# Kernel optimization log

Measured on AMD Instinct MI355X. Metric: run time of the kernel, lower is better.

The kernel has to match this reference:

```python
import jax, jax.numpy as jnp
import numpy as np
import math

HEAD_DIM = 128
DEPTH = 12
LAMBDA_INIT = 0.8 - 0.6 * math.exp(-0.3 * DEPTH)
EPS = 1e-5
SCALE = 1.0 / math.sqrt(HEAD_DIM / 2)


def setup_inputs() -> dict:
    key = jax.random.key(0)
    ks = jax.random.split(key, 8)
    b, t, d = 2, 4096, 2048
    return {
        "x": jax.random.normal(ks[0], (b, t, d), dtype=jnp.float32),
        "wq": jax.random.normal(ks[1], (d, HEAD_DIM), dtype=jnp.float32) * 0.02,
        "wk": jax.random.normal(ks[2], (d, HEAD_DIM), dtype=jnp.float32) * 0.02,
        "wv": jax.random.normal(ks[3], (d, HEAD_DIM), dtype=jnp.float32) * 0.02,
        "lambda_q1": jax.random.normal(ks[4], (HEAD_DIM // 2,), dtype=jnp.float32) * 0.1,
        "lambda_q2": jax.random.normal(ks[5], (HEAD_DIM // 2,), dtype=jnp.float32) * 0.1,
        "lambda_k1": jax.random.normal(ks[6], (HEAD_DIM // 2,), dtype=jnp.float32) * 0.1,
        "lambda_k2": jax.random.normal(ks[7], (HEAD_DIM // 2,), dtype=jnp.float32) * 0.1,
        "ln_weight": jnp.ones((HEAD_DIM,), dtype=jnp.float32),
    }


def reference(x, wq, wk, wv, lambda_q1, lambda_q2, lambda_k1, lambda_k2, ln_weight):
    b, t, d = x.shape
    q = x @ wq  # [b,t,hd]
    k = x @ wk
    v = x @ wv
    h = HEAD_DIM // 2
    q1, q2 = q[..., :h], q[..., h:]
    k1, k2 = k[..., :h], k[..., h:]
    # causal mask: True where attention is disallowed (strictly upper triangle)
    causal = jnp.triu(jnp.ones((t, t), dtype=bool), k=1)
    neg_inf = jnp.float32(-jnp.inf)

    def masked_softmax(qh, kh):
        scores = jnp.einsum('btd,bsd->bts', qh, kh) * SCALE
        scores = jnp.where(causal, neg_inf, scores)
        return jax.nn.softmax(scores, axis=-1)

    a1 = masked_softmax(q1, k1)
    a2 = masked_softmax(q2, k2)
    lmbda = (jnp.exp(jnp.sum(lambda_q1 * lambda_k1))
             - jnp.exp(jnp.sum(lambda_q2 * lambda_k2))
             + LAMBDA_INIT)
    diffattn = jnp.einsum('bts,bsd->btd', a1 - lmbda * a2, v)
    rms = jnp.sqrt(jnp.mean(diffattn * diffattn, axis=-1, keepdims=True) + EPS)
    out = (1.0 - LAMBDA_INIT) * (diffattn / rms * ln_weight)
    return out
```

## Files before the change

### kernel.cpp

```cpp
#include <hip/hip_runtime.h>
#include <stdint.h>

#define T_SEQ 4096
#define NB 2
#define D_MODEL 2048
#define HD 128

typedef __attribute__((ext_vector_type(4)))  float f32x4;
typedef __attribute__((ext_vector_type(16))) float f32x16;
typedef __attribute__((ext_vector_type(8)))  short bf16x8;
typedef __attribute__((ext_vector_type(4)))  unsigned u32x4;

#define LAMBDA_INIT 0.7836057665316244f
#define OUT_SCALE   0.21639423346837556f

__device__ __forceinline__ unsigned short f2bf(float f) {
  unsigned int u = __float_as_uint(f);
  u += 0x7FFFu + ((u >> 16) & 1u);
  return (unsigned short)(u >> 16);
}
__device__ __forceinline__ float bf2f(unsigned short h) {
  return __uint_as_float(((unsigned int)h) << 16);
}
__device__ __forceinline__ unsigned cvt_pk_bf16(float a, float b) {
  unsigned r;
  asm("v_cvt_pk_bf16_f32 %0, %1, %2" : "=v"(r) : "v"(a), "v"(b));
  return r;
}
__device__ __forceinline__ void gload16(const void* g, void* l) {
  __builtin_amdgcn_global_load_lds(
      (const __attribute__((address_space(1))) unsigned int*)g,
      (__attribute__((address_space(3))) unsigned int*)l, 16, 0, 0);
}

__global__ __launch_bounds__(256) void wtrans(
    const float* __restrict__ wq, const float* __restrict__ wk,
    const float* __restrict__ wv, unsigned short* __restrict__ wT)
{
  const int which = blockIdx.y;
  const int s = blockIdx.x;
  const float* w = (which == 0) ? wq : ((which == 1) ? wk : wv);
  const float scale = (which == 0) ? 0.125f : 1.0f;
  const int tid = threadIdx.x;
  #pragma unroll
  for (int j = 0; j < 4; ++j) {
    int cell = j * 256 + tid;
    int q = cell >> 7, n = cell & 127;
    int kb = s * 64 + q * 8;
    float v[8];
    #pragma unroll
    for (int e = 0; e < 8; ++e) v[e] = w[(size_t)(kb + e) * HD + n] * scale;
    u32x4 pk = { cvt_pk_bf16(v[0], v[1]), cvt_pk_bf16(v[2], v[3]),
                 cvt_pk_bf16(v[4], v[5]), cvt_pk_bf16(v[6], v[7]) };
    *reinterpret_cast<u32x4*>(&wT[(size_t)(which * 32 + s) * 8192 + (size_t)cell * 8]) = pk;
  }
}

__global__ __launch_bounds__(512, 1) void qkv_part(
    const float* __restrict__ x, const unsigned short* __restrict__ wT,
    float* __restrict__ P)
{
  __shared__ __align__(16) char lds[4][32768];
  const int tid = threadIdx.x, lane = tid & 63, wid = tid >> 6;
  const int bid = blockIdx.x;
  const int ks = bid & 1;
  const int mt = bid >> 1;
  const int wm = wid >> 1, wn = wid & 1;
  const int fr = lane & 15, fq = lane >> 4;
  const int m0 = mt * 64;

  const float* xbase = x + (size_t)m0 * D_MODEL + ks * 1024;
  const unsigned short* wbase = wT + (size_t)(ks * 16) * 8192;

  f32x4 acc[3][4];
  #pragma unroll
  for (int ty = 0; ty < 3; ++ty)
    #pragma unroll
    for (int j = 0; j < 4; ++j) acc[ty][j] = (f32x4){0.f, 0.f, 0.f, 0.f};

#define DMA(t) do {                                                        \
    char* As_ = &lds[(t) & 3][0];                                          \
    char* Bs_ = &lds[(t) & 3][8192];                                       \
    const int k0_ = (t) * 32;                                              \
    {                                                                      \
      int c = wid * 64 + lane;                                             \
      int row = c >> 3, kcp = c & 7;                                       \
      gload16(xbase + (size_t)row * D_MODEL + k0_ + ((kcp ^ (row & 7)) << 2), \
              As_ + wid * 1024);                                           \
    }                                                                      \
    _Pragma("unroll")                                                      \
    for (int ty = 0; ty < 3; ++ty) {                                       \
      const unsigned short* bs_ = wbase + (size_t)ty * 262144              \
                                + (size_t)((t) >> 1) * 8192                \
                                + (size_t)((t) & 1) * 4096;                \
      gload16(bs_ + (size_t)wid * 512 + (size_t)lane * 8,                  \
              Bs_ + (size_t)ty * 8192 + wid * 1024);                       \
    }                                                                      \
  } while (0)

#define STEP(t, VMIMM) do {                                                \
    asm volatile("s_waitcnt vmcnt(" VMIMM ")" ::: "memory");               \
    __builtin_amdgcn_s_barrier();                                          \
    __builtin_amdgcn_sched_barrier(0);                                     \
    if ((t) + 3 < 32) DMA((t) + 3);                                        \
    __builtin_amdgcn_sched_barrier(0);                                     \
    const char* Ac_ = &lds[(t) & 3][0];                                    \
    const char* Bc_ = &lds[(t) & 3][8192];                                 \
    bf16x8 af_;                                                            \
    {                                                                      \
      int row = wm * 16 + fr;                                              \
      int p1 = (2 * fq) ^ (row & 7), p2 = (2 * fq + 1) ^ (row & 7);        \
      f32x4 lo = *reinterpret_cast<const f32x4*>(Ac_ + (row * 8 + p1) * 16); \
      f32x4 hi = *reinterpret_cast<const f32x4*>(Ac_ + (row * 8 + p2) * 16); \
      u32x4 pk = { cvt_pk_bf16(lo[0], lo[1]), cvt_pk_bf16(lo[2], lo[3]),   \
                   cvt_pk_bf16(hi[0], hi[1]), cvt_pk_bf16(hi[2], hi[3]) }; \
      af_ = *reinterpret_cast<bf16x8*>(&pk);                               \
    }                                                                      \
    _Pragma("unroll")                                                      \
    for (int ty = 0; ty < 3; ++ty)                                         \
      _Pragma("unroll")                                                    \
      for (int ni = 0; ni < 4; ++ni) {                                     \
        int n = wn * 64 + ni * 16 + fr;                                    \
        bf16x8 bf_ = *reinterpret_cast<const bf16x8*>(                     \
            Bc_ + (size_t)ty * 8192 + (fq * 128 + n) * 16);                \
        acc[ty][ni] = __builtin_amdgcn_mfma_f32_16x16x32_bf16(af_, bf_, acc[ty][ni], 0, 0, 0); \
      }                                                                    \
  } while (0)

  DMA(0); DMA(1); DMA(2);
  #pragma unroll 1
  for (int t = 0; t < 30; ++t) STEP(t, "8");
  STEP(30, "4");
  STEP(31, "0");
#undef STEP
#undef DMA

  #pragma unroll
  for (int ty = 0; ty < 3; ++ty) {
    float* pp = P + ((size_t)(ks * 3 + ty) * 8192 + m0) * 128;
    #pragma unroll
    for (int ni = 0; ni < 4; ++ni)
      #pragma unroll
      for (int r = 0; r < 4; ++r)
        pp[(size_t)(wm * 16 + fq * 4 + r) * 128 + wn * 64 + ni * 16 + fr]
            = acc[ty][ni][r];
  }
}

__global__ __launch_bounds__(256) void qkv_merge(
    const float* __restrict__ P,
    unsigned short* __restrict__ qb, unsigned short* __restrict__ kS,
    unsigned short* __restrict__ vS)
{
  const int gid = blockIdx.x * 256 + threadIdx.x;
  const size_t e8 = (size_t)gid * 8;
  const int type = (int)(e8 >> 20);
  const int rem  = (int)(e8 & 1048575);
  const int m = rem >> 7, n0 = rem & 127;
  const float* p0 = P + (size_t)type * 1048576 + rem;
  const float* p1 = p0 + (size_t)3 * 1048576;
  f32x4 a0 = *reinterpret_cast<const f32x4*>(p0);
  f32x4 a1 = *reinterpret_cast<const f32x4*>(p0 + 4);
  f32x4 b0 = *reinterpret_cast<const f32x4*>(p1);
  f32x4 b1 = *reinterpret_cast<const f32x4*>(p1 + 4);
  float s[8];
  #pragma unroll
  for (int j = 0; j < 4; ++j) { s[j] = a0[j] + b0[j]; s[4 + j] = a1[j] + b1[j]; }
  u32x4 pk = { cvt_pk_bf16(s[0], s[1]), cvt_pk_bf16(s[2], s[3]),
               cvt_pk_bf16(s[4], s[5]), cvt_pk_bf16(s[6], s[7]) };

  const int bb = m >> 12, tt = m & 4095;
  const int kt = tt >> 5, kvl = tt & 31;
  if (type == 0) {
    *reinterpret_cast<u32x4*>(&qb[(size_t)m * HD + n0]) = pk;
  } else if (type == 1) {
    int g = n0 >> 6, hl = n0 & 63;
    int ksf = hl >> 4, r8 = (hl >> 3) & 1;
    size_t idx = ((((((size_t)bb * 128 + kt) * 2 + g) * 4) + ksf) << 9)
               + (size_t)(kvl + 32 * r8) * 8;
    *reinterpret_cast<u32x4*>(&kS[idx]) = pk;
  } else {
    int f = kvl >> 4, r8v = (kvl >> 3) & 1, e = kvl & 7;
    #pragma unroll
    for (int j = 0; j < 8; ++j) {
      int n = n0 + j;
      int vcb = n >> 5;
      size_t idx = (((((size_t)bb * 128 + kt) * 8) + vcb * 2 + f) << 9)
                 + (size_t)((n & 31) + 32 * r8v) * 8 + e;
      vS[idx] = f2bf(s[j]);
    }
  }
}

template<int LOG2S>
__global__ __launch_bounds__(256, 2) void diff_attn_part(
    const unsigned short* __restrict__ qb, const unsigned short* __restrict__ kS,
    const unsigned short* __restrict__ vS,
    unsigned short* __restrict__ po, float* __restrict__ pm, float* __restrict__ pl)
{
  constexpr int S = 1 << LOG2S;
  const int tid = threadIdx.x, lane = tid & 63, wid = tid >> 6;
  const int wave_id = blockIdx.x * 4 + wid;
  const int sp = wave_id & (S - 1);
  const int g  = (wave_id >> LOG2S) & 1;
  const int qt_raw = (wave_id >> (LOG2S + 1)) & 127;
  const int b  = wave_id >> (LOG2S + 8);
  const int qt = 127 - qt_raw;
  const int slot = (((b * 128 + qt) * 2 + g) << LOG2S) + sp;
  const int lq = lane & 31, lh = lane >> 5;
  const int q0 = qt * 32;
  const int n  = qt + 1;
  const int kt0 = (n * sp) >> LOG2S;
  const int kt1 = (n * (sp + 1)) >> LOG2S;

  bf16x8 qf[4];
  const unsigned short* qp = qb + ((size_t)b * T_SEQ + q0 + lq) * HD + g * 64 + lh * 8;
  #pragma unroll
  for (int ks = 0; ks < 4; ++ks) qf[ks] = *reinterpret_cast<const bf16x8*>(qp + ks * 16);

  f32x16 acc[4];
  #pragma unroll
  for (int v = 0; v < 4; ++v)
    #pragma unroll
    for (int r = 0; r < 16; ++r) acc[v][r] = 0.f;
  float mrun = -1e30f, lrun = 0.f;

  const unsigned short* kbase = kS + ((size_t)(b * 128) * 2 + g) * 4 * 512 + lane * 8;
  const unsigned short* vbase = vS + (size_t)(b * 128) * 8 * 512 + lane * 8;
  #define KFRAG(kt, ks) (kbase + ((size_t)(kt) * 8 + (ks)) * 512)
  #define VFRAG(kt, f)  (vbase + ((size_t)(kt) * 8 + (f)) * 512)

  bf16x8 kf[4];
  if (kt0 < kt1) {
    #pragma unroll
    for (int ks = 0; ks < 4; ++ks)
      kf[ks] = *reinterpret_cast<const bf16x8*>(KFRAG(kt0, ks));
  }

  for (int kt = kt0; kt < kt1; ++kt) {
    bf16x8 vfa[4], vfb[4];
    #pragma unroll
    for (int vcb = 0; vcb < 4; ++vcb) {
      vfa[vcb] = *reinterpret_cast<const bf16x8*>(VFRAG(kt, vcb * 2));
      vfb[vcb] = *reinterpret_cast<const bf16x8*>(VFRAG(kt, vcb * 2 + 1));
    }
    bf16x8 kfn[4];
    const bool more = (kt + 1 < kt1);
    if (more) {
      #pragma unroll
      for (int ks = 0; ks < 4; ++ks)
        kfn[ks] = *reinterpret_cast<const bf16x8*>(KFRAG(kt + 1, ks));
    }
    f32x16 sc;
    #pragma unroll
    for (int r = 0; r < 16; ++r) sc[r] = 0.f;
    #pragma unroll
    for (int ks = 0; ks < 4; ++ks)
      sc = __builtin_amdgcn_mfma_f32_32x32x16_bf16(kf[ks], qf[ks], sc, 0, 0, 0);

    float p[16];
    if (kt == n - 1) {
      #pragma unroll
      for (int r = 0; r < 16; ++r) {
        int rloc = (r & 3) + 8 * (r >> 2) + 4 * lh;
        p[r] = (rloc > lq) ? -1e30f : sc[r];
      }
    } else {
      #pragma unroll
      for (int r = 0; r < 16; ++r) p[r] = sc[r];
    }
    float t16[16];
    #pragma unroll
    for (int r = 0; r < 16; ++r) t16[r] = p[r];
    #pragma unroll
    for (int st = 8; st >= 1; st >>= 1)
      #pragma unroll
      for (int r = 0; r < 8; ++r)
        if (r < st) t16[r] = fmaxf(t16[r], t16[r + st]);
    float pmax = fmaxf(t16[0], __shfl_xor(t16[0], 32));
    if (__any(pmax > mrun + 8.f)) {
      float mn = fmaxf(mrun, pmax);
      float al = __expf(mrun - mn);
      lrun *= al;
      #pragma unroll
      for (int v = 0; v < 4; ++v)
        #pragma unroll
        for (int r = 0; r < 16; ++r) acc[v][r] *= al;
      mrun = mn;
    }
    float psum;
    {
      float s16[16];
      #pragma unroll
      for (int r = 0; r < 16; ++r) { p[r] = __expf(p[r] - mrun); s16[r] = p[r]; }
      #pragma unroll
      for (int st = 8; st >= 1; st >>= 1)
        #pragma unroll
        for (int r = 0; r < 8; ++r)
          if (r < st) s16[r] += s16[r + st];
      psum = s16[0];
    }
    lrun += psum + __shfl_xor(psum, 32);

    unsigned A0 = cvt_pk_bf16(p[0],  p[1]),  A1 = cvt_pk_bf16(p[2],  p[3]);
    unsigned A2 = cvt_pk_bf16(p[4],  p[5]),  A3 = cvt_pk_bf16(p[6],  p[7]);
    unsigned A4 = cvt_pk_bf16(p[8],  p[9]),  A5 = cvt_pk_bf16(p[10], p[11]);
    unsigned A6 = cvt_pk_bf16(p[12], p[13]), A7 = cvt_pk_bf16(p[14], p[15]);
    unsigned pA0 = (unsigned)__shfl_xor((int)A0, 32);
    unsigned pA1 = (unsigned)__shfl_xor((int)A1, 32);
    unsigned pA2 = (unsigned)__shfl_xor((int)A2, 32);
    unsigned pA3 = (unsigned)__shfl_xor((int)A3, 32);
    unsigned pA4 = (unsigned)__shfl_xor((int)A4, 32);
    unsigned pA5 = (unsigned)__shfl_xor((int)A5, 32);
    unsigned pA6 = (unsigned)__shfl_xor((int)A6, 32);
    unsigned pA7 = (unsigned)__shfl_xor((int)A7, 32);
    u32x4 w0, w1;
    w0[0] = lh ? pA2 : A0;  w0[1] = lh ? pA3 : A1;
    w0[2] = lh ? A2  : pA0; w0[3] = lh ? A3  : pA1;
    w1[0] = lh ? pA6 : A4;  w1[1] = lh ? pA7 : A5;
    w1[2] = lh ? A6  : pA4; w1[3] = lh ? A7  : pA5;
    bf16x8 pb0 = *reinterpret_cast<bf16x8*>(&w0);
    bf16x8 pb1 = *reinterpret_cast<bf16x8*>(&w1);
    #pragma unroll
    for (int vcb = 0; vcb < 4; ++vcb) {
      acc[vcb] = __builtin_amdgcn_mfma_f32_32x32x16_bf16(vfa[vcb], pb0, acc[vcb], 0, 0, 0);
      acc[vcb] = __builtin_amdgcn_mfma_f32_32x32x16_bf16(vfb[vcb], pb1, acc[vcb], 0, 0, 0);
    }
    if (more) {
      #pragma unroll
      for (int ks = 0; ks < 4; ++ks) kf[ks] = kfn[ks];
    }
  }
  #undef KFRAG
  #undef VFRAG
  const size_t pbase = (size_t)slot * (HD * 32);
  #pragma unroll
  for (int vcb = 0; vcb < 4; ++vcb)
    #pragma unroll
    for (int r = 0; r < 16; ++r) {
      int vc = vcb * 32 + (r & 3) + 8 * (r >> 2) + 4 * lh;
      po[pbase + (size_t)vc * 32 + lq] = f2bf(acc[vcb][r]);
    }
  if (lane < 32) {
    pm[slot * 32 + lq] = mrun;
    pl[slot * 32 + lq] = lrun;
  }
}

template<int LOG2S>
__global__ __launch_bounds__(256) void diff_merge(
    const unsigned short* __restrict__ po, const float* __restrict__ pm,
    const float* __restrict__ pl,
    const float* __restrict__ lq1, const float* __restrict__ lq2,
    const float* __restrict__ lk1, const float* __restrict__ lk2,
    const float* __restrict__ lnw, float* __restrict__ out)
{
  constexpr int S = 1 << LOG2S;
  __shared__ float red[4][32];
  const int tid = threadIdx.x, lane = tid & 63, wid = tid >> 6;
  const int q = tid & 31, vg = tid >> 5;
  const int bq = blockIdx.x;
  const int b = bq >> 7, qt = bq & 127;

  float la = lq1[lane] * lk1[lane];
  float lb = lq2[lane] * lk2[lane];
  #pragma unroll
  for (int off = 32; off >= 1; off >>= 1) {
    la += __shfl_xor(la, off);
    lb += __shfl_xor(lb, off);
  }
  const float lam = __expf(la) - __expf(lb) + LAMBDA_INIT;

  const int p1 = (bq * 2 + 0) * S;
  const int p2 = (bq * 2 + 1) * S;
  float w1[S], w2[S];
  {
    float ms[S];
    #pragma unroll
    for (int s = 0; s < S; ++s) ms[s] = pm[(p1 + s) * 32 + q];
    float M = ms[0];
    #pragma unroll
    for (int s = 1; s < S; ++s) M = fmaxf(M, ms[s]);
    float L = 0.f;
    #pragma unroll
    for (int s = 0; s < S; ++s) { w1[s] = __expf(ms[s] - M); L += w1[s] * pl[(p1 + s) * 32 + q]; }
    float inv = 1.f / L;
    #pragma unroll
    for (int s = 0; s < S; ++s) w1[s] *= inv;
  }
  {
    float ms[S];
    #pragma unroll
    for (int s = 0; s < S; ++s) ms[s] = pm[(p2 + s) * 32 + q];
    float M = ms[0];
    #pragma unroll
    for (int s = 1; s < S; ++s) M = fmaxf(M, ms[s]);
    float L = 0.f;
    #pragma unroll
    for (int s = 0; s < S; ++s) { w2[s] = __expf(ms[s] - M); L += w2[s] * pl[(p2 + s) * 32 + q]; }
    float inv = lam / L;
    #pragma unroll
    for (int s = 0; s < S; ++s) w2[s] *= inv;
  }
  float d[16], ss = 0.f;
  #pragma unroll
  for (int i = 0; i < 16; ++i) {
    int vc = vg * 16 + i;
    float a1 = 0.f, a2 = 0.f;
    #pragma unroll
    for (int s = 0; s < S; ++s) {
      a1 += w1[s] * bf2f(po[(size_t)(p1 + s) * (HD * 32) + (size_t)vc * 32 + q]);
      a2 += w2[s] * bf2f(po[(size_t)(p2 + s) * (HD * 32) + (size_t)vc * 32 + q]);
    }
    d[i] = a1 - a2;
    ss += d[i] * d[i];
  }
  ss += __shfl_xor(ss, 32);
  if (lane < 32) red[wid][q] = ss;
  __syncthreads();
  float tot = red[0][q] + red[1][q] + red[2][q] + red[3][q];
  float rinv = 1.f / sqrtf(tot * (1.0f / HD) + 1e-5f);
  float* op = out + ((size_t)b * T_SEQ + qt * 32 + q) * HD + vg * 16;
  #pragma unroll
  for (int i = 0; i < 16; ++i) op[i] = OUT_SCALE * d[i] * rinv * lnw[vg * 16 + i];
}

extern "C" void kernel_launch(void* const* d_in, const int* in_sizes, int n_in,
                              void* d_out, int out_size, void* d_ws, size_t ws_size,
                              hipStream_t stream) {
  const float* x   = (const float*)d_in[0];
  const float* wq  = (const float*)d_in[1];
  const float* wk  = (const float*)d_in[2];
  const float* wv  = (const float*)d_in[3];
  const float* lq1 = (const float*)d_in[4];
  const float* lq2 = (const float*)d_in[5];
  const float* lk1 = (const float*)d_in[6];
  const float* lk2 = (const float*)d_in[7];
  const float* lnw = (const float*)d_in[8];
  float* out = (float*)d_out;

  const size_t N = (size_t)NB * T_SEQ * HD;
  const size_t WTN = (size_t)3 * 32 * 8192;
  const size_t PB  = (size_t)2 * 3 * 8192 * 128 * 4;
  int log2S = 3;
  size_t parts = 0, region = 0;
  for (;; --log2S) {
    parts = ((size_t)NB * 128 * 2) << log2S;
    size_t pob = parts * (HD * 32) * 2;
    size_t rmin = PB + WTN * 2;
    region = (pob > rmin) ? pob : rmin;
    size_t need = 3 * N * 2 + region + parts * 32 * 8;
    if (need <= ws_size || log2S == 0) break;
  }

  unsigned short* qb = (unsigned short*)d_ws;
  unsigned short* kS = qb + N;
  unsigned short* vS = kS + N;
  unsigned short* po = vS + N;
  float* Ppart = (float*)po;
  unsigned short* wT = (unsigned short*)((char*)po + region) - WTN;
  float* pm = (float*)((char*)po + region);
  float* pl = pm + parts * 32;

  wtrans<<<dim3(32, 3), 256, 0, stream>>>(wq, wk, wv, wT);
  qkv_part<<<dim3(256), 512, 0, stream>>>(x, wT, Ppart);
  qkv_merge<<<dim3(1536), 256, 0, stream>>>(Ppart, qb, kS, vS);
  const int ablocks = (int)(parts / 4);
  switch (log2S) {
    case 3:
      diff_attn_part<3><<<dim3(ablocks), 256, 0, stream>>>(qb, kS, vS, po, pm, pl);
      diff_merge<3><<<dim3(NB * 128), 256, 0, stream>>>(po, pm, pl, lq1, lq2, lk1, lk2, lnw, out);
      break;
    case 2:
      diff_attn_part<2><<<dim3(ablocks), 256, 0, stream>>>(qb, kS, vS, po, pm, pl);
      diff_merge<2><<<dim3(NB * 128), 256, 0, stream>>>(po, pm, pl, lq1, lq2, lk1, lk2, lnw, out);
      break;
    case 1:
      diff_attn_part<1><<<dim3(ablocks), 256, 0, stream>>>(qb, kS, vS, po, pm, pl);
      diff_merge<1><<<dim3(NB * 128), 256, 0, stream>>>(po, pm, pl, lq1, lq2, lk1, lk2, lnw, out);
      break;
    default:
      diff_attn_part<0><<<dim3(ablocks), 256, 0, stream>>>(qb, kS, vS, po, pm, pl);
      diff_merge<0><<<dim3(NB * 128), 256, 0, stream>>>(po, pm, pl, lq1, lq2, lk1, lk2, lnw, out);
      break;
  }
}
```

Baseline: 78.55 us.

## Drop split-K in QKV projection and write bf16 Q/K/V layouts directly

```diff
diff --git a/kernel.cpp b/kernel.cpp
--- a/kernel.cpp
+++ b/kernel.cpp
@@ -58,54 +58,56 @@
 
 __global__ __launch_bounds__(512, 1) void qkv_part(
     const float* __restrict__ x, const unsigned short* __restrict__ wT,
-    float* __restrict__ P)
+    unsigned short* __restrict__ qb, unsigned short* __restrict__ kS,
+    unsigned short* __restrict__ vS)
 {
-  __shared__ __align__(16) char lds[4][32768];
+  __shared__ __align__(16) char lds[4][28672];
   const int tid = threadIdx.x, lane = tid & 63, wid = tid >> 6;
-  const int bid = blockIdx.x;
-  const int ks = bid & 1;
-  const int mt = bid >> 1;
-  const int wm = wid >> 1, wn = wid & 1;
+  const int mt = blockIdx.x;
+  const int wm = wid >> 2, wn = wid & 3;
   const int fr = lane & 15, fq = lane >> 4;
-  const int m0 = mt * 64;
-
-  const float* xbase = x + (size_t)m0 * D_MODEL + ks * 1024;
-  const unsigned short* wbase = wT + (size_t)(ks * 16) * 8192;
-
-  f32x4 acc[3][4];
-  #pragma unroll
-  for (int ty = 0; ty < 3; ++ty)
-    #pragma unroll
-    for (int j = 0; j < 4; ++j) acc[ty][j] = (f32x4){0.f, 0.f, 0.f, 0.f};
+  const int m0 = mt * 32;
+
+  const float* xbase = x + (size_t)m0 * D_MODEL;
+
+  f32x4 acc[6];
+  #pragma unroll
+  for (int j = 0; j < 6; ++j) acc[j] = (f32x4){0.f, 0.f, 0.f, 0.f};
 
 #define DMA(t) do {                                                        \
     char* As_ = &lds[(t) & 3][0];                                          \
-    char* Bs_ = &lds[(t) & 3][8192];                                       \
+    char* Bs_ = &lds[(t) & 3][4096];                                       \
     const int k0_ = (t) * 32;                                              \
-    {                                                                      \
+    if (wid < 4) {                                                         \
       int c = wid * 64 + lane;                                             \
-      int row = c >> 3, kcp = c & 7;                                       \
-      gload16(xbase + (size_t)row * D_MODEL + k0_ + ((kcp ^ (row & 7)) << 2), \
+      int row = c >> 3, kc = c & 7;                                        \
+      gload16(xbase + (size_t)row * D_MODEL + k0_ + ((kc ^ (row & 7)) << 2), \
               As_ + wid * 1024);                                           \
     }                                                                      \
+    const unsigned short* sb_ = wT + (size_t)((t) >> 1) * 8192             \
+                              + (size_t)((t) & 1) * 4096 + (size_t)lane * 8; \
     _Pragma("unroll")                                                      \
-    for (int ty = 0; ty < 3; ++ty) {                                       \
-      const unsigned short* bs_ = wbase + (size_t)ty * 262144              \
-                                + (size_t)((t) >> 1) * 8192                \
-                                + (size_t)((t) & 1) * 4096;                \
-      gload16(bs_ + (size_t)wid * 512 + (size_t)lane * 8,                  \
-              Bs_ + (size_t)ty * 8192 + wid * 1024);                       \
+    for (int j = 0; j < 3; ++j) {                                          \
+      int c = wid * 3 + j;                                                 \
+      int ty = c >> 3, cc = c & 7;                                         \
+      gload16(sb_ + (size_t)ty * 262144 + (size_t)cc * 512,                \
+              Bs_ + ty * 8192 + cc * 1024);                                \
     }                                                                      \
   } while (0)
 
-#define STEP(t, VMIMM) do {                                                \
-    asm volatile("s_waitcnt vmcnt(" VMIMM ")" ::: "memory");               \
+#define WAITV(a, b) do {                                                   \
+    if (wid < 4) asm volatile("s_waitcnt vmcnt(" a ")" ::: "memory");      \
+    else         asm volatile("s_waitcnt vmcnt(" b ")" ::: "memory");      \
+  } while (0)
+
+#define STEP(t, VA, VB) do {                                               \
+    WAITV(VA, VB);                                                         \
     __builtin_amdgcn_s_barrier();                                          \
     __builtin_amdgcn_sched_barrier(0);                                     \
-    if ((t) + 3 < 32) DMA((t) + 3);                                        \
+    if ((t) + 3 < 64) DMA((t) + 3);                                        \
     __builtin_amdgcn_sched_barrier(0);                                     \
     const char* Ac_ = &lds[(t) & 3][0];                                    \
-    const char* Bc_ = &lds[(t) & 3][8192];                                 \
+    const char* Bc_ = &lds[(t) & 3][4096];                                 \
     bf16x8 af_;                                                            \
     {                                                                      \
       int row = wm * 16 + fr;                                              \
@@ -117,77 +119,49 @@
       af_ = *reinterpret_cast<bf16x8*>(&pk);                               \
     }                                                                      \
     _Pragma("unroll")                                                      \
-    for (int ty = 0; ty < 3; ++ty)                                         \
-      _Pragma("unroll")                                                    \
-      for (int ni = 0; ni < 4; ++ni) {                                     \
-        int n = wn * 64 + ni * 16 + fr;                                    \
-        bf16x8 bf_ = *reinterpret_cast<const bf16x8*>(                     \
-            Bc_ + (size_t)ty * 8192 + (fq * 128 + n) * 16);                \
-        acc[ty][ni] = __builtin_amdgcn_mfma_f32_16x16x32_bf16(af_, bf_, acc[ty][ni], 0, 0, 0); \
-      }                                                                    \
+    for (int ni = 0; ni < 6; ++ni) {                                       \
+      int nb = wn * 96 + ni * 16;                                          \
+      int ty = nb >> 7, nnb = nb & 127;                                    \
+      bf16x8 bf_ = *reinterpret_cast<const bf16x8*>(                       \
+          Bc_ + (size_t)ty * 8192 + (fq * 128 + nnb + fr) * 16);           \
+      acc[ni] = __builtin_amdgcn_mfma_f32_16x16x32_bf16(af_, bf_, acc[ni], 0, 0, 0); \
+    }                                                                      \
   } while (0)
 
   DMA(0); DMA(1); DMA(2);
   #pragma unroll 1
-  for (int t = 0; t < 30; ++t) STEP(t, "8");
-  STEP(30, "4");
-  STEP(31, "0");
+  for (int t = 0; t < 62; ++t) STEP(t, "8", "6");
+  STEP(62, "4", "3");
+  STEP(63, "0", "0");
 #undef STEP
+#undef WAITV
 #undef DMA
 
   #pragma unroll
-  for (int ty = 0; ty < 3; ++ty) {
-    float* pp = P + ((size_t)(ks * 3 + ty) * 8192 + m0) * 128;
-    #pragma unroll
-    for (int ni = 0; ni < 4; ++ni)
-      #pragma unroll
-      for (int r = 0; r < 4; ++r)
-        pp[(size_t)(wm * 16 + fq * 4 + r) * 128 + wn * 64 + ni * 16 + fr]
-            = acc[ty][ni][r];
-  }
-}
-
-__global__ __launch_bounds__(256) void qkv_merge(
-    const float* __restrict__ P,
-    unsigned short* __restrict__ qb, unsigned short* __restrict__ kS,
-    unsigned short* __restrict__ vS)
-{
-  const int gid = blockIdx.x * 256 + threadIdx.x;
-  const size_t e8 = (size_t)gid * 8;
-  const int type = (int)(e8 >> 20);
-  const int rem  = (int)(e8 & 1048575);
-  const int m = rem >> 7, n0 = rem & 127;
-  const float* p0 = P + (size_t)type * 1048576 + rem;
-  const float* p1 = p0 + (size_t)3 * 1048576;
-  f32x4 a0 = *reinterpret_cast<const f32x4*>(p0);
-  f32x4 a1 = *reinterpret_cast<const f32x4*>(p0 + 4);
-  f32x4 b0 = *reinterpret_cast<const f32x4*>(p1);
-  f32x4 b1 = *reinterpret_cast<const f32x4*>(p1 + 4);
-  float s[8];
-  #pragma unroll
-  for (int j = 0; j < 4; ++j) { s[j] = a0[j] + b0[j]; s[4 + j] = a1[j] + b1[j]; }
-  u32x4 pk = { cvt_pk_bf16(s[0], s[1]), cvt_pk_bf16(s[2], s[3]),
-               cvt_pk_bf16(s[4], s[5]), cvt_pk_bf16(s[6], s[7]) };
-
-  const int bb = m >> 12, tt = m & 4095;
-  const int kt = tt >> 5, kvl = tt & 31;
-  if (type == 0) {
-    *reinterpret_cast<u32x4*>(&qb[(size_t)m * HD + n0]) = pk;
-  } else if (type == 1) {
-    int g = n0 >> 6, hl = n0 & 63;
-    int ksf = hl >> 4, r8 = (hl >> 3) & 1;
-    size_t idx = ((((((size_t)bb * 128 + kt) * 2 + g) * 4) + ksf) << 9)
-               + (size_t)(kvl + 32 * r8) * 8;
-    *reinterpret_cast<u32x4*>(&kS[idx]) = pk;
-  } else {
-    int f = kvl >> 4, r8v = (kvl >> 3) & 1, e = kvl & 7;
-    #pragma unroll
-    for (int j = 0; j < 8; ++j) {
-      int n = n0 + j;
-      int vcb = n >> 5;
-      size_t idx = (((((size_t)bb * 128 + kt) * 8) + vcb * 2 + f) << 9)
-                 + (size_t)((n & 31) + 32 * r8v) * 8 + e;
-      vS[idx] = f2bf(s[j]);
+  for (int ni = 0; ni < 6; ++ni) {
+    int nb = wn * 96 + ni * 16;
+    int ty = nb >> 7, nn = (nb & 127) + fr;
+    #pragma unroll
+    for (int r = 0; r < 4; ++r) {
+      int m = m0 + wm * 16 + fq * 4 + r;
+      float vv = acc[ni][r];
+      int bb = m >> 12, tt = m & 4095;
+      int kt = tt >> 5, kvl = tt & 31;
+      if (ty == 0) {
+        qb[(size_t)m * HD + nn] = f2bf(vv);
+      } else if (ty == 1) {
+        int g = nn >> 6, hl = nn & 63;
+        int ksf = hl >> 4, r8 = (hl >> 3) & 1, e = hl & 7;
+        size_t idx = ((((((size_t)bb * 128 + kt) * 2 + g) * 4) + ksf) << 9)
+                   + (size_t)(kvl + 32 * r8) * 8 + e;
+        kS[idx] = f2bf(vv);
+      } else {
+        int f = kvl >> 4, r8v = (kvl >> 3) & 1, e = kvl & 7;
+        int vcb = nn >> 5;
+        size_t idx = (((((size_t)bb * 128 + kt) * 8) + vcb * 2 + f) << 9)
+                   + (size_t)((nn & 31) + 32 * r8v) * 8 + e;
+        vS[idx] = f2bf(vv);
+      }
     }
   }
 }
@@ -441,13 +415,12 @@
 
   const size_t N = (size_t)NB * T_SEQ * HD;
   const size_t WTN = (size_t)3 * 32 * 8192;
-  const size_t PB  = (size_t)2 * 3 * 8192 * 128 * 4;
   int log2S = 3;
   size_t parts = 0, region = 0;
   for (;; --log2S) {
     parts = ((size_t)NB * 128 * 2) << log2S;
     size_t pob = parts * (HD * 32) * 2;
-    size_t rmin = PB + WTN * 2;
+    size_t rmin = WTN * 2;
     region = (pob > rmin) ? pob : rmin;
     size_t need = 3 * N * 2 + region + parts * 32 * 8;
     if (need <= ws_size || log2S == 0) break;
@@ -457,14 +430,12 @@
   unsigned short* kS = qb + N;
   unsigned short* vS = kS + N;
   unsigned short* po = vS + N;
-  float* Ppart = (float*)po;
   unsigned short* wT = (unsigned short*)((char*)po + region) - WTN;
   float* pm = (float*)((char*)po + region);
   float* pl = pm + parts * 32;
 
   wtrans<<<dim3(32, 3), 256, 0, stream>>>(wq, wk, wv, wT);
-  qkv_part<<<dim3(256), 512, 0, stream>>>(x, wT, Ppart);
-  qkv_merge<<<dim3(1536), 256, 0, stream>>>(Ppart, qb, kS, vS);
+  qkv_part<<<dim3(256), 512, 0, stream>>>(x, wT, qb, kS, vS);
   const int ablocks = (int)(parts / 4);
   switch (log2S) {
     case 3:
```

New measurement: 80.37 us. +2.3%, slower.
